# Kernel optimization log

Hardware: AMD Instinct MI355X
Metric: run time of the kernel (lower is better)

## Reference

```python
import jax, jax.numpy as jnp
import numpy as np

N = 50000      # nodes
E = 800000     # edges (before self-loops)
F_IN = 128     # num_features
H = 4          # heads
C = 64         # hidden_channels
HC = H * C     # 256
NEG_SLOPE = 0.2


def setup_inputs() -> dict:
    key = jax.random.key(0)
    ks = jax.random.split(key, 20)
    x = jax.random.normal(ks[0], (N, F_IN), dtype=jnp.float32)
    edge_index = jax.random.randint(ks[1], (2, E), 0, N, dtype=jnp.int32)
    s = 0.05
    inp = {"x": x, "edge_index": edge_index}
    dims_in = [F_IN, HC, HC, HC]
    for l in range(4):
        kW, ka, kb = jax.random.split(ks[2 + l], 3)
        inp[f"W{l+1}"] = jax.random.normal(kW, (dims_in[l], HC), dtype=jnp.float32) * s
        inp[f"a_src{l+1}"] = jax.random.normal(ka, (H, C), dtype=jnp.float32) * s
        inp[f"a_dst{l+1}"] = jax.random.normal(kb, (H, C), dtype=jnp.float32) * s
        inp[f"b{l+1}"] = jnp.zeros((HC,), dtype=jnp.float32)
    return inp


def gat_conv(x, src, dst, W, a_src, a_dst, b):
    # x: [N, F_in] -> h: [N, H, C]
    h = (x @ W).reshape(N, H, C)
    es = jnp.sum(h * a_src, axis=-1)  # [N, H] per-node source logits
    ed = jnp.sum(h * a_dst, axis=-1)  # [N, H]
    e = jax.nn.leaky_relu(es[src] + ed[dst], NEG_SLOPE)  # [Etot, H]
    m = jax.ops.segment_max(e, dst, num_segments=N)      # per-dst max
    m = jnp.where(jnp.isfinite(m), m, 0.0)
    ex = jnp.exp(e - m[dst])
    denom = jax.ops.segment_sum(ex, dst, num_segments=N)
    alpha = ex / (denom[dst] + 1e-16)                     # edge softmax
    out = jax.ops.segment_sum(alpha[:, :, None] * h[src], dst, num_segments=N)
    return out.reshape(N, HC) + b


def reference(x, edge_index,
              W1, a_src1, a_dst1, b1,
              W2, a_src2, a_dst2, b2,
              W3, a_src3, a_dst3, b3,
              W4, a_src4, a_dst4, b4):
    loop = jnp.arange(N, dtype=edge_index.dtype)
    src = jnp.concatenate([edge_index[0], loop])  # add self-loops (PyG default)
    dst = jnp.concatenate([edge_index[1], loop])
    x1 = jax.nn.relu(gat_conv(x, src, dst, W1, a_src1, a_dst1, b1))
    x2 = jax.nn.relu(gat_conv(x1, src, dst, W2, a_src2, a_dst2, b2))
    x3 = jax.nn.relu(gat_conv(x2 + x1, src, dst, W3, a_src3, a_dst3, b3))
    x4 = jax.nn.relu(gat_conv(x2 + x3, src, dst, W4, a_src4, a_dst4, b4))
    # NOTE: source code calls conv4 again (not conv5) -- reproduced faithfully
    x5 = gat_conv(x4 + x3, src, dst, W4, a_src4, a_dst4, b4)
    return x5
```

## Files before the change

### kernel.cpp

```cpp
#include <hip/hip_runtime.h>
#include <hip/hip_bf16.h>

#define N_NODES 50000
#define E_EDGES 800000
#define ETOT (E_EDGES + N_NODES)
#define HC 256
#define NHEAD 4
#define CHAN 64
#define NEG 0.2f
#define NBLK ((N_NODES + 1023) / 1024)

typedef _Float16 half8 __attribute__((ext_vector_type(8)));
typedef _Float16 half4v __attribute__((ext_vector_type(4)));
typedef float float4v __attribute__((ext_vector_type(4)));


__global__ void count_kernel(const int* __restrict__ ei, int* __restrict__ counts) {
    int i = blockIdx.x * blockDim.x + threadIdx.x;
    if (i >= ETOT) return;
    int dst = (i < E_EDGES) ? ei[E_EDGES + i] : (i - E_EDGES);
    atomicAdd(&counts[dst], 1);
}

__global__ __launch_bounds__(256) void blocksum_kernel(const int* __restrict__ counts,
                                                       int* __restrict__ blocksums) {
    __shared__ int s[4];
    int b = blockIdx.x, tid = threadIdx.x;
    int base = b * 1024;
    int sum = 0;
    #pragma unroll
    for (int r = 0; r < 4; ++r) {
        int idx = base + r * 256 + tid;
        sum += (idx < N_NODES) ? counts[idx] : 0;
    }
    #pragma unroll
    for (int m = 1; m < 64; m <<= 1) sum += __shfl_xor(sum, m, 64);
    if ((tid & 63) == 0) s[tid >> 6] = sum;
    __syncthreads();
    if (tid == 0) blocksums[b] = s[0] + s[1] + s[2] + s[3];
}

__global__ __launch_bounds__(64) void blockscan_kernel(int* __restrict__ blocksums) {
    int tid = threadIdx.x;
    int v = (tid < NBLK) ? blocksums[tid] : 0;
    #pragma unroll
    for (int off = 1; off < 64; off <<= 1) {
        int t = __shfl_up(v, off, 64);
        if (tid >= off) v += t;
    }
    if (tid < NBLK) blocksums[tid] = v;
}

__global__ __launch_bounds__(1024) void scatter_scan_kernel(const int* __restrict__ counts,
                                                            const int* __restrict__ blocksums,
                                                            int* __restrict__ offsets,
                                                            int* __restrict__ cursor) {
    __shared__ int s[1024];
    int b = blockIdx.x, tid = threadIdx.x;
    int idx = b * 1024 + tid;
    int v = (idx < N_NODES) ? counts[idx] : 0;
    s[tid] = v;
    __syncthreads();
    for (int off = 1; off < 1024; off <<= 1) {
        int t = (tid >= off) ? s[tid - off] : 0;
        __syncthreads();
        s[tid] += t;
        __syncthreads();
    }
    int excl = s[tid] - v + (b > 0 ? blocksums[b - 1] : 0);
    if (idx < N_NODES) { offsets[idx] = excl; cursor[idx] = excl; }
    if (idx == N_NODES - 1) offsets[N_NODES] = excl + v;
}

__global__ void fill_kernel(const int* __restrict__ ei, int* __restrict__ cursor,
                            int* __restrict__ csr_src) {
    int i = blockIdx.x * blockDim.x + threadIdx.x;
    if (i >= ETOT) return;
    int src, dst;
    if (i < E_EDGES) { src = ei[i]; dst = ei[E_EDGES + i]; }
    else             { src = i - E_EDGES; dst = src; }
    int pos = atomicAdd(&cursor[dst], 1);
    csr_src[pos] = src;
}


__global__ void wsplit_kernel(const float* __restrict__ W, _Float16* __restrict__ Wth,
                              _Float16* __restrict__ Wtl, int K) {
    int id = blockIdx.x * 256 + threadIdx.x;
    if (id >= K * 256) return;
    int n = id & 255, k = id >> 8;
    float w = W[(size_t)k * 256 + n];
    _Float16 h = (_Float16)w;
    _Float16 l = (_Float16)(w - (float)h);
    Wth[(size_t)n * K + k] = h;
    Wtl[(size_t)n * K + k] = l;
}


#define LDK 40

__global__ __launch_bounds__(256) void gemm_mfma_kernel(
        const float* __restrict__ A1, const float* __restrict__ A2,
        const _Float16* __restrict__ Wth, const _Float16* __restrict__ Wtl,
        const float* __restrict__ a_src, const float* __restrict__ a_dst,
        _Float16* __restrict__ H16, float* __restrict__ es, float* __restrict__ ed,
        int M, int K) {
    __shared__ _Float16 Ah[64][LDK];
    __shared__ _Float16 Al[64][LDK];
    __shared__ _Float16 Bh[256][LDK];
    __shared__ _Float16 Bl[256][LDK];

    int tid = threadIdx.x;
    int m0 = blockIdx.x * 64;
    int w = tid >> 6, lane = tid & 63;
    int rn = w * 64;
    int fr = lane & 15;
    int q  = lane >> 4;
    int fk = q * 8;

    int ar = tid >> 3;
    int ak = (tid & 7) * 4;
    int wr = tid >> 2;
    int wk = (tid & 3) * 8;

    float4v acc[4][4];
    #pragma unroll
    for (int i = 0; i < 4; ++i)
        #pragma unroll
        for (int j = 0; j < 4; ++j)
            acc[i][j] = (float4v){0.f, 0.f, 0.f, 0.f};

    bool has2 = (A2 != nullptr);
    float4 pa1[2], pa2[2];
    half8 pbh[4], pbl[4];

    auto load_tile = [&](int k0) {
        #pragma unroll
        for (int g = 0; g < 2; ++g) {
            int row = m0 + g * 32 + ar;
            pa1[g] = make_float4(0.f, 0.f, 0.f, 0.f);
            pa2[g] = make_float4(0.f, 0.f, 0.f, 0.f);
            if (row < M) {
                pa1[g] = *(const float4*)(A1 + (size_t)row * K + k0 + ak);
                if (has2) pa2[g] = *(const float4*)(A2 + (size_t)row * K + k0 + ak);
            }
        }
        #pragma unroll
        for (int g = 0; g < 4; ++g) {
            int r = g * 64 + wr;
            pbh[g] = *(const half8*)(Wth + (size_t)r * K + k0 + wk);
            pbl[g] = *(const half8*)(Wtl + (size_t)r * K + k0 + wk);
        }
    };

    load_tile(0);
    for (int k0 = 0; k0 < K; k0 += 32) {
        #pragma unroll
        for (int g = 0; g < 2; ++g) {
            int r = g * 32 + ar;
            float4 v;
            v.x = pa1[g].x + pa2[g].x; v.y = pa1[g].y + pa2[g].y;
            v.z = pa1[g].z + pa2[g].z; v.w = pa1[g].w + pa2[g].w;
            half4v hv = {(_Float16)v.x, (_Float16)v.y, (_Float16)v.z, (_Float16)v.w};
            half4v lv = {(_Float16)(v.x - (float)hv[0]), (_Float16)(v.y - (float)hv[1]),
                         (_Float16)(v.z - (float)hv[2]), (_Float16)(v.w - (float)hv[3])};
            *(half4v*)&Ah[r][ak] = hv;
            *(half4v*)&Al[r][ak] = lv;
        }
        #pragma unroll
        for (int g = 0; g < 4; ++g) {
            int r = g * 64 + wr;
            *(half8*)&Bh[r][wk] = pbh[g];
            *(half8*)&Bl[r][wk] = pbl[g];
        }
        __syncthreads();
        if (k0 + 32 < K) load_tile(k0 + 32);
        half8 afh[4], afl[4], bfh[4], bfl[4];
        #pragma unroll
        for (int t = 0; t < 4; ++t) {
            afh[t] = *(const half8*)&Ah[t * 16 + fr][fk];
            afl[t] = *(const half8*)&Al[t * 16 + fr][fk];
            bfh[t] = *(const half8*)&Bh[rn + t * 16 + fr][fk];
            bfl[t] = *(const half8*)&Bl[rn + t * 16 + fr][fk];
        }
        #pragma unroll
        for (int tm = 0; tm < 4; ++tm)
            #pragma unroll
            for (int tn = 0; tn < 4; ++tn) {
                float4v c = acc[tm][tn];
                c = __builtin_amdgcn_mfma_f32_16x16x32_f16(afl[tm], bfh[tn], c, 0, 0, 0);
                c = __builtin_amdgcn_mfma_f32_16x16x32_f16(afh[tm], bfl[tn], c, 0, 0, 0);
                c = __builtin_amdgcn_mfma_f32_16x16x32_f16(afh[tm], bfh[tn], c, 0, 0, 0);
                acc[tm][tn] = c;
            }
        __syncthreads();
    }

    float asv[4], adv[4];
    #pragma unroll
    for (int tn = 0; tn < 4; ++tn) {
        asv[tn] = a_src[w * CHAN + tn * 16 + fr];
        adv[tn] = a_dst[w * CHAN + tn * 16 + fr];
    }
    #pragma unroll
    for (int tm = 0; tm < 4; ++tm) {
        #pragma unroll
        for (int i = 0; i < 4; ++i) {
            int row = m0 + tm * 16 + q * 4 + i;
            float ps = 0.f, pd = 0.f;
            #pragma unroll
            for (int tn = 0; tn < 4; ++tn) {
                float hv = acc[tm][tn][i];
                ps += hv * asv[tn];
                pd += hv * adv[tn];
                if (row < M)
                    H16[(size_t)row * HC + rn + tn * 16 + fr] = (_Float16)hv;
            }
            #pragma unroll
            for (int msk = 1; msk < 16; msk <<= 1) {
                ps += __shfl_xor(ps, msk, 64);
                pd += __shfl_xor(pd, msk, 64);
            }
            if (fr == 0 && row < M) {
                es[row * NHEAD + w] = ps;
                ed[row * NHEAD + w] = pd;
            }
        }
    }
}


__global__ __launch_bounds__(256) void gat_aggregate_kernel(
        const _Float16* __restrict__ H16, const float* __restrict__ es, const float* __restrict__ ed,
        const int* __restrict__ offsets, const int* __restrict__ csr_src,
        const float* __restrict__ bias, float* __restrict__ out, int do_relu) {
    __shared__ float alpha_lds[4][256];
    int tid = threadIdx.x;
    int w = tid >> 6, lane = tid & 63;
    int n = blockIdx.x * 4 + w;
    int off = offsets[n];
    int deg = offsets[n + 1] - off;
    float4 edv = *(const float4*)(ed + (size_t)n * 4);

    if (deg <= 64) {
        int sreg = 0;
        float4 e4 = make_float4(-1e30f, -1e30f, -1e30f, -1e30f);
        if (lane < deg) {
            sreg = csr_src[off + lane];
            float4 esv = *(const float4*)(es + (size_t)sreg * 4);
            e4.x = esv.x + edv.x; e4.y = esv.y + edv.y;
            e4.z = esv.z + edv.z; e4.w = esv.w + edv.w;
            e4.x = (e4.x > 0.f) ? e4.x : NEG * e4.x;
            e4.y = (e4.y > 0.f) ? e4.y : NEG * e4.y;
            e4.z = (e4.z > 0.f) ? e4.z : NEG * e4.z;
            e4.w = (e4.w > 0.f) ? e4.w : NEG * e4.w;
        }
        float4 m4 = e4;
        #pragma unroll
        for (int msk = 1; msk < 64; msk <<= 1) {
            m4.x = fmaxf(m4.x, __shfl_xor(m4.x, msk, 64));
            m4.y = fmaxf(m4.y, __shfl_xor(m4.y, msk, 64));
            m4.z = fmaxf(m4.z, __shfl_xor(m4.z, msk, 64));
            m4.w = fmaxf(m4.w, __shfl_xor(m4.w, msk, 64));
        }
        float4 ex4 = make_float4(0.f, 0.f, 0.f, 0.f);
        if (lane < deg) {
            ex4.x = __expf(e4.x - m4.x); ex4.y = __expf(e4.y - m4.y);
            ex4.z = __expf(e4.z - m4.z); ex4.w = __expf(e4.w - m4.w);
        }
        float4 l4 = ex4;
        #pragma unroll
        for (int msk = 1; msk < 64; msk <<= 1) {
            l4.x += __shfl_xor(l4.x, msk, 64);
            l4.y += __shfl_xor(l4.y, msk, 64);
            l4.z += __shfl_xor(l4.z, msk, 64);
            l4.w += __shfl_xor(l4.w, msk, 64);
        }
        float4 a4;
        a4.x = ex4.x / (l4.x + 1e-16f);
        a4.y = ex4.y / (l4.y + 1e-16f);
        a4.z = ex4.z / (l4.z + 1e-16f);
        a4.w = ex4.w / (l4.w + 1e-16f);
        *(float4*)&alpha_lds[w][lane * 4] = a4;

        int hl = lane & 31, side = lane >> 5;
        int hd = hl >> 3;
        float av[8] = {0.f, 0.f, 0.f, 0.f, 0.f, 0.f, 0.f, 0.f};
        #pragma unroll 2
        for (int j = side; j < deg; j += 2) {
            int s = __shfl(sreg, j, 64);
            float al = alpha_lds[w][j * 4 + hd];
            half8 hv = *(const half8*)(H16 + (size_t)s * HC + hl * 8);
            #pragma unroll
            for (int c = 0; c < 8; ++c) av[c] += al * (float)hv[c];
        }
        #pragma unroll
        for (int c = 0; c < 8; ++c) av[c] += __shfl_xor(av[c], 32, 64);
        if (side == 0) {
            float4 b0 = *(const float4*)(bias + hl * 8);
            float4 b1 = *(const float4*)(bias + hl * 8 + 4);
            float4 o0 = make_float4(av[0] + b0.x, av[1] + b0.y, av[2] + b0.z, av[3] + b0.w);
            float4 o1 = make_float4(av[4] + b1.x, av[5] + b1.y, av[6] + b1.z, av[7] + b1.w);
            if (do_relu) {
                o0.x = fmaxf(o0.x, 0.f); o0.y = fmaxf(o0.y, 0.f);
                o0.z = fmaxf(o0.z, 0.f); o0.w = fmaxf(o0.w, 0.f);
                o1.x = fmaxf(o1.x, 0.f); o1.y = fmaxf(o1.y, 0.f);
                o1.z = fmaxf(o1.z, 0.f); o1.w = fmaxf(o1.w, 0.f);
            }
            *(float4*)(out + (size_t)n * HC + hl * 8) = o0;
            *(float4*)(out + (size_t)n * HC + hl * 8 + 4) = o1;
        }
        return;
    }

    int head = lane >> 4;
    float4 acc0 = make_float4(0.f, 0.f, 0.f, 0.f);
    float m[4] = {-1e30f, -1e30f, -1e30f, -1e30f};
    float l[4] = {0.f, 0.f, 0.f, 0.f};
    for (int base = 0; base < deg; base += 64) {
        int j = base + lane;
        if (j < deg) {
            int s = csr_src[off + j];
            float4 esv = *(const float4*)(es + (size_t)s * 4);
            float e[4] = {esv.x + edv.x, esv.y + edv.y, esv.z + edv.z, esv.w + edv.w};
            #pragma unroll
            for (int h = 0; h < 4; ++h) {
                e[h] = (e[h] > 0.f) ? e[h] : NEG * e[h];
                float M2 = fmaxf(m[h], e[h]);
                l[h] = l[h] * __expf(m[h] - M2) + __expf(e[h] - M2);
                m[h] = M2;
            }
        }
    }
    #pragma unroll
    for (int msk = 1; msk < 64; msk <<= 1) {
        #pragma unroll
        for (int h = 0; h < 4; ++h) {
            float mo = __shfl_xor(m[h], msk, 64);
            float lo = __shfl_xor(l[h], msk, 64);
            float M2 = fmaxf(m[h], mo);
            l[h] = l[h] * __expf(m[h] - M2) + lo * __expf(mo - M2);
            m[h] = M2;
        }
    }
    float fm = m[head];
    float fr2 = 1.f / (l[head] + 1e-16f);
    float edh = ((const float*)&edv)[head];
    for (int j = 0; j < deg; ++j) {
        int s = csr_src[off + j];
        float e = es[(size_t)s * 4 + head] + edh;
        e = (e > 0.f) ? e : NEG * e;
        float alpha = __expf(e - fm) * fr2;
        half4v h0 = *(const half4v*)(H16 + (size_t)s * HC + lane * 4);
        acc0.x += alpha * (float)h0[0]; acc0.y += alpha * (float)h0[1];
        acc0.z += alpha * (float)h0[2]; acc0.w += alpha * (float)h0[3];
    }
    float4 b4 = *(const float4*)(bias + lane * 4);
    float4 o;
    o.x = acc0.x + b4.x; o.y = acc0.y + b4.y;
    o.z = acc0.z + b4.z; o.w = acc0.w + b4.w;
    if (do_relu) {
        o.x = fmaxf(o.x, 0.f); o.y = fmaxf(o.y, 0.f);
        o.z = fmaxf(o.z, 0.f); o.w = fmaxf(o.w, 0.f);
    }
    *(float4*)(out + (size_t)n * HC + lane * 4) = o;
}


extern "C" void kernel_launch(void* const* d_in, const int* in_sizes, int n_in,
                              void* d_out, int out_size, void* d_ws, size_t ws_size,
                              hipStream_t stream) {
    const float* x  = (const float*)d_in[0];
    const int*   ei = (const int*)d_in[1];
    const float *W[5], *Asrc[5], *Adst[5], *Bs[5];
    for (int l = 0; l < 4; ++l) {
        W[l]    = (const float*)d_in[2 + l * 4];
        Asrc[l] = (const float*)d_in[3 + l * 4];
        Adst[l] = (const float*)d_in[4 + l * 4];
        Bs[l]   = (const float*)d_in[5 + l * 4];
    }
    W[4] = W[3]; Asrc[4] = Asrc[3]; Adst[4] = Adst[3]; Bs[4] = Bs[3];

    char* ws = (char*)d_ws;
    size_t off = 0;
    auto alloc = [&](size_t bytes) -> void* {
        void* p = ws + off;
        off += (bytes + 255) & ~(size_t)255;
        return p;
    };
    _Float16* h16  = (_Float16*)alloc((size_t)N_NODES * HC * 2);
    float* xa      = (float*)alloc((size_t)N_NODES * HC * 4);
    float* xb      = (float*)alloc((size_t)N_NODES * HC * 4);
    float* xc      = (float*)alloc((size_t)N_NODES * HC * 4);
    float* es      = (float*)alloc((size_t)N_NODES * 4 * 4);
    float* ed      = (float*)alloc((size_t)N_NODES * 4 * 4);
    int*   counts  = (int*)alloc((size_t)N_NODES * 4);
    int*   offsets = (int*)alloc((size_t)(N_NODES + 1) * 4);
    int*   cursor  = (int*)alloc((size_t)N_NODES * 4);
    int*   csr_src = (int*)alloc((size_t)ETOT * 4);
    int*   blocksums = (int*)alloc((size_t)NBLK * 4);
    _Float16 *Wth[5], *Wtl[5];
    int Ks[4] = {128, 256, 256, 256};
    for (int l = 0; l < 4; ++l) {
        Wth[l] = (_Float16*)alloc((size_t)256 * Ks[l] * 2);
        Wtl[l] = (_Float16*)alloc((size_t)256 * Ks[l] * 2);
    }
    Wth[4] = Wth[3]; Wtl[4] = Wtl[3];

    hipMemsetAsync(counts, 0, (size_t)N_NODES * 4, stream);
    count_kernel<<<(ETOT + 255) / 256, 256, 0, stream>>>(ei, counts);
    blocksum_kernel<<<NBLK, 256, 0, stream>>>(counts, blocksums);
    blockscan_kernel<<<1, 64, 0, stream>>>(blocksums);
    scatter_scan_kernel<<<NBLK, 1024, 0, stream>>>(counts, blocksums, offsets, cursor);
    fill_kernel<<<(ETOT + 255) / 256, 256, 0, stream>>>(ei, cursor, csr_src);
    for (int l = 0; l < 4; ++l)
        wsplit_kernel<<<(Ks[l] * 256 + 255) / 256, 256, 0, stream>>>(W[l], Wth[l], Wtl[l], Ks[l]);

    auto layer = [&](const float* in1, const float* in2, int K, int l, float* outp, int relu) {
        gemm_mfma_kernel<<<(N_NODES + 63) / 64, 256, 0, stream>>>(
            in1, in2, Wth[l], Wtl[l], Asrc[l], Adst[l], h16, es, ed, N_NODES, K);
        gat_aggregate_kernel<<<N_NODES / 4, 256, 0, stream>>>(h16, es, ed, offsets, csr_src,
                                                              Bs[l], outp, relu);
    };

    float* out = (float*)d_out;
    layer(x,  nullptr, 128, 0, xa, 1);
    layer(xa, nullptr, 256, 1, xb, 1);
    layer(xb, xa,      256, 2, xc, 1);
    layer(xb, xc,      256, 3, xa, 1);
    layer(xa, xc,      256, 4, out, 0);
}
```

Baseline: 811.2 us.

## Store intermediate activations in fp16 and drop low-part MFMA for them

Intermediate layer outputs are now written as fp16 instead of fp32, which halves activation write and read traffic. The GEMM takes fp16 A inputs directly, adds residual pairs in fp16, and skips the A-low split MFMA for layers 2-5. The input x is pre-split into hi/lo fp16 by a new kernel so layer 1 keeps its extra precision. This trades some accuracy, from fp16 activations and fp16 residual sums, for less memory traffic and a third fewer MFMAs in most layers.

Result: no change. 798.2 us (-1.6%).

```diff
diff --git a/kernel.cpp b/kernel.cpp
--- a/kernel.cpp
+++ b/kernel.cpp
@@ -96,11 +96,22 @@
     Wtl[(size_t)n * K + k] = l;
 }
 
+__global__ void xsplit_kernel(const float* __restrict__ x, _Float16* __restrict__ xh,
+                              _Float16* __restrict__ xl, int total) {
+    int id = blockIdx.x * 256 + threadIdx.x;
+    if (id >= total) return;
+    float v = x[id];
+    _Float16 h = (_Float16)v;
+    xh[id] = h;
+    xl[id] = (_Float16)(v - (float)h);
+}
+
 
 #define LDK 40
 
 __global__ __launch_bounds__(256) void gemm_mfma_kernel(
-        const float* __restrict__ A1, const float* __restrict__ A2,
+        const _Float16* __restrict__ A1h, const _Float16* __restrict__ A1l,
+        const _Float16* __restrict__ A2h,
         const _Float16* __restrict__ Wth, const _Float16* __restrict__ Wtl,
         const float* __restrict__ a_src, const float* __restrict__ a_dst,
         _Float16* __restrict__ H16, float* __restrict__ es, float* __restrict__ ed,
@@ -118,11 +129,12 @@
     int q  = lane >> 4;
     int fk = q * 8;
 
-    int ar = tid >> 3;
-    int ak = (tid & 7) * 4;
     int wr = tid >> 2;
     int wk = (tid & 3) * 8;
 
+    bool has_lo = (A1l != nullptr);
+    bool has2   = (A2h != nullptr);
+
     float4v acc[4][4];
     #pragma unroll
     for (int i = 0; i < 4; ++i)
@@ -130,20 +142,19 @@
         for (int j = 0; j < 4; ++j)
             acc[i][j] = (float4v){0.f, 0.f, 0.f, 0.f};
 
-    bool has2 = (A2 != nullptr);
-    float4 pa1[2], pa2[2];
-    half8 pbh[4], pbl[4];
+    half8 pa, pal, pbh[4], pbl[4];
 
     auto load_tile = [&](int k0) {
-        #pragma unroll
-        for (int g = 0; g < 2; ++g) {
-            int row = m0 + g * 32 + ar;
-            pa1[g] = make_float4(0.f, 0.f, 0.f, 0.f);
-            pa2[g] = make_float4(0.f, 0.f, 0.f, 0.f);
-            if (row < M) {
-                pa1[g] = *(const float4*)(A1 + (size_t)row * K + k0 + ak);
-                if (has2) pa2[g] = *(const float4*)(A2 + (size_t)row * K + k0 + ak);
-            }
+        int row = m0 + wr;
+        pa  = (half8)(_Float16)0;
+        pal = (half8)(_Float16)0;
+        if (row < M) {
+            pa = *(const half8*)(A1h + (size_t)row * K + k0 + wk);
+            if (has2) {
+                half8 u = *(const half8*)(A2h + (size_t)row * K + k0 + wk);
+                pa = pa + u;
+            }
+            if (has_lo) pal = *(const half8*)(A1l + (size_t)row * K + k0 + wk);
         }
         #pragma unroll
         for (int g = 0; g < 4; ++g) {
@@ -155,18 +166,8 @@
 
     load_tile(0);
     for (int k0 = 0; k0 < K; k0 += 32) {
-        #pragma unroll
-        for (int g = 0; g < 2; ++g) {
-            int r = g * 32 + ar;
-            float4 v;
-            v.x = pa1[g].x + pa2[g].x; v.y = pa1[g].y + pa2[g].y;
-            v.z = pa1[g].z + pa2[g].z; v.w = pa1[g].w + pa2[g].w;
-            half4v hv = {(_Float16)v.x, (_Float16)v.y, (_Float16)v.z, (_Float16)v.w};
-            half4v lv = {(_Float16)(v.x - (float)hv[0]), (_Float16)(v.y - (float)hv[1]),
-                         (_Float16)(v.z - (float)hv[2]), (_Float16)(v.w - (float)hv[3])};
-            *(half4v*)&Ah[r][ak] = hv;
-            *(half4v*)&Al[r][ak] = lv;
-        }
+        *(half8*)&Ah[wr][wk] = pa;
+        if (has_lo) *(half8*)&Al[wr][wk] = pal;
         #pragma unroll
         for (int g = 0; g < 4; ++g) {
             int r = g * 64 + wr;
@@ -175,20 +176,29 @@
         }
         __syncthreads();
         if (k0 + 32 < K) load_tile(k0 + 32);
-        half8 afh[4], afl[4], bfh[4], bfl[4];
+        half8 afh[4], bfh[4], bfl[4];
         #pragma unroll
         for (int t = 0; t < 4; ++t) {
             afh[t] = *(const half8*)&Ah[t * 16 + fr][fk];
-            afl[t] = *(const half8*)&Al[t * 16 + fr][fk];
             bfh[t] = *(const half8*)&Bh[rn + t * 16 + fr][fk];
             bfl[t] = *(const half8*)&Bl[rn + t * 16 + fr][fk];
         }
+        if (has_lo) {
+            half8 afl[4];
+            #pragma unroll
+            for (int t = 0; t < 4; ++t) afl[t] = *(const half8*)&Al[t * 16 + fr][fk];
+            #pragma unroll
+            for (int tm = 0; tm < 4; ++tm)
+                #pragma unroll
+                for (int tn = 0; tn < 4; ++tn)
+                    acc[tm][tn] = __builtin_amdgcn_mfma_f32_16x16x32_f16(
+                        afl[tm], bfh[tn], acc[tm][tn], 0, 0, 0);
+        }
         #pragma unroll
         for (int tm = 0; tm < 4; ++tm)
             #pragma unroll
             for (int tn = 0; tn < 4; ++tn) {
                 float4v c = acc[tm][tn];
-                c = __builtin_amdgcn_mfma_f32_16x16x32_f16(afl[tm], bfh[tn], c, 0, 0, 0);
                 c = __builtin_amdgcn_mfma_f32_16x16x32_f16(afh[tm], bfl[tn], c, 0, 0, 0);
                 c = __builtin_amdgcn_mfma_f32_16x16x32_f16(afh[tm], bfh[tn], c, 0, 0, 0);
                 acc[tm][tn] = c;
@@ -233,7 +243,8 @@
 __global__ __launch_bounds__(256) void gat_aggregate_kernel(
         const _Float16* __restrict__ H16, const float* __restrict__ es, const float* __restrict__ ed,
         const int* __restrict__ offsets, const int* __restrict__ csr_src,
-        const float* __restrict__ bias, float* __restrict__ out, int do_relu) {
+        const float* __restrict__ bias, _Float16* __restrict__ out16,
+        float* __restrict__ out32, int do_relu) {
     __shared__ float alpha_lds[4][256];
     int tid = threadIdx.x;
     int w = tid >> 6, lane = tid & 63;
@@ -299,16 +310,21 @@
         if (side == 0) {
             float4 b0 = *(const float4*)(bias + hl * 8);
             float4 b1 = *(const float4*)(bias + hl * 8 + 4);
-            float4 o0 = make_float4(av[0] + b0.x, av[1] + b0.y, av[2] + b0.z, av[3] + b0.w);
-            float4 o1 = make_float4(av[4] + b1.x, av[5] + b1.y, av[6] + b1.z, av[7] + b1.w);
-            if (do_relu) {
-                o0.x = fmaxf(o0.x, 0.f); o0.y = fmaxf(o0.y, 0.f);
-                o0.z = fmaxf(o0.z, 0.f); o0.w = fmaxf(o0.w, 0.f);
-                o1.x = fmaxf(o1.x, 0.f); o1.y = fmaxf(o1.y, 0.f);
-                o1.z = fmaxf(o1.z, 0.f); o1.w = fmaxf(o1.w, 0.f);
-            }
-            *(float4*)(out + (size_t)n * HC + hl * 8) = o0;
-            *(float4*)(out + (size_t)n * HC + hl * 8 + 4) = o1;
+            float o[8] = {av[0] + b0.x, av[1] + b0.y, av[2] + b0.z, av[3] + b0.w,
+                          av[4] + b1.x, av[5] + b1.y, av[6] + b1.z, av[7] + b1.w};
+            if (do_relu)
+                #pragma unroll
+                for (int c = 0; c < 8; ++c) o[c] = fmaxf(o[c], 0.f);
+            if (out16) {
+                half8 ov = {(_Float16)o[0], (_Float16)o[1], (_Float16)o[2], (_Float16)o[3],
+                            (_Float16)o[4], (_Float16)o[5], (_Float16)o[6], (_Float16)o[7]};
+                *(half8*)(out16 + (size_t)n * HC + hl * 8) = ov;
+            } else {
+                *(float4*)(out32 + (size_t)n * HC + hl * 8) =
+                    make_float4(o[0], o[1], o[2], o[3]);
+                *(float4*)(out32 + (size_t)n * HC + hl * 8 + 4) =
+                    make_float4(o[4], o[5], o[6], o[7]);
+            }
         }
         return;
     }
@@ -356,14 +372,16 @@
         acc0.z += alpha * (float)h0[2]; acc0.w += alpha * (float)h0[3];
     }
     float4 b4 = *(const float4*)(bias + lane * 4);
-    float4 o;
-    o.x = acc0.x + b4.x; o.y = acc0.y + b4.y;
-    o.z = acc0.z + b4.z; o.w = acc0.w + b4.w;
-    if (do_relu) {
-        o.x = fmaxf(o.x, 0.f); o.y = fmaxf(o.y, 0.f);
-        o.z = fmaxf(o.z, 0.f); o.w = fmaxf(o.w, 0.f);
-    }
-    *(float4*)(out + (size_t)n * HC + lane * 4) = o;
+    float o[4] = {acc0.x + b4.x, acc0.y + b4.y, acc0.z + b4.z, acc0.w + b4.w};
+    if (do_relu)
+        #pragma unroll
+        for (int c = 0; c < 4; ++c) o[c] = fmaxf(o[c], 0.f);
+    if (out16) {
+        half4v ov = {(_Float16)o[0], (_Float16)o[1], (_Float16)o[2], (_Float16)o[3]};
+        *(half4v*)(out16 + (size_t)n * HC + lane * 4) = ov;
+    } else {
+        *(float4*)(out32 + (size_t)n * HC + lane * 4) = make_float4(o[0], o[1], o[2], o[3]);
+    }
 }
 
 
@@ -389,9 +407,12 @@
         return p;
     };
     _Float16* h16  = (_Float16*)alloc((size_t)N_NODES * HC * 2);
-    float* xa      = (float*)alloc((size_t)N_NODES * HC * 4);
-    float* xb      = (float*)alloc((size_t)N_NODES * HC * 4);
-    float* xc      = (float*)alloc((size_t)N_NODES * HC * 4);
+    _Float16* xa   = (_Float16*)alloc((size_t)N_NODES * HC * 2);
+    _Float16* xb   = (_Float16*)alloc((size_t)N_NODES * HC * 2);
+    _Float16* xc   = (_Float16*)alloc((size_t)N_NODES * HC * 2);
+    _Float16* xd   = (_Float16*)alloc((size_t)N_NODES * HC * 2);
+    _Float16* xh   = (_Float16*)alloc((size_t)N_NODES * 128 * 2);
+    _Float16* xl   = (_Float16*)alloc((size_t)N_NODES * 128 * 2);
     float* es      = (float*)alloc((size_t)N_NODES * 4 * 4);
     float* ed      = (float*)alloc((size_t)N_NODES * 4 * 4);
     int*   counts  = (int*)alloc((size_t)N_NODES * 4);
@@ -415,18 +436,20 @@
     fill_kernel<<<(ETOT + 255) / 256, 256, 0, stream>>>(ei, cursor, csr_src);
     for (int l = 0; l < 4; ++l)
         wsplit_kernel<<<(Ks[l] * 256 + 255) / 256, 256, 0, stream>>>(W[l], Wth[l], Wtl[l], Ks[l]);
-
-    auto layer = [&](const float* in1, const float* in2, int K, int l, float* outp, int relu) {
+    xsplit_kernel<<<(N_NODES * 128 + 255) / 256, 256, 0, stream>>>(x, xh, xl, N_NODES * 128);
+
+    auto layer = [&](const _Float16* a1h, const _Float16* a1l, const _Float16* a2h,
+                     int K, int l, _Float16* o16, float* o32, int relu) {
         gemm_mfma_kernel<<<(N_NODES + 63) / 64, 256, 0, stream>>>(
-            in1, in2, Wth[l], Wtl[l], Asrc[l], Adst[l], h16, es, ed, N_NODES, K);
-        gat_aggregate_kernel<<<N_NODES / 4, 256, 0, stream>>>(h16, es, ed, offsets, csr_src,
-                                                              Bs[l], outp, relu);
+            a1h, a1l, a2h, Wth[l], Wtl[l], Asrc[l], Adst[l], h16, es, ed, N_NODES, K);
+        gat_aggregate_kernel<<<N_NODES / 4, 256, 0, stream>>>(
+            h16, es, ed, offsets, csr_src, Bs[l], o16, o32, relu);
     };
 
     float* out = (float*)d_out;
-    layer(x,  nullptr, 128, 0, xa, 1);
-    layer(xa, nullptr, 256, 1, xb, 1);
-    layer(xb, xa,      256, 2, xc, 1);
-    layer(xb, xc,      256, 3, xa, 1);
-    layer(xa, xc,      256, 4, out, 0);
-}
+    layer(xh, xl,      nullptr, 128, 0, xa, nullptr, 1);
+    layer(xa, nullptr, nullptr, 256, 1, xb, nullptr, 1);
+    layer(xb, nullptr, xa,      256, 2, xc, nullptr, 1);
+    layer(xb, nullptr, xc,      256, 3, xd, nullptr, 1);
+    layer(xd, nullptr, xc,      256, 4, nullptr, out, 0);
+}
```
